# Performance work log

Measured on AMD Instinct MI355X. Metric: run time of the kernel, lower is better.

Reference implementation:

```python
import jax, jax.numpy as jnp
import numpy as np

B = 8
H_IN, W_IN = 448, 448
STRIDE = 32
NUM_CLASSES = 20
CONF_THRESH = 0.01
NMS_THRESH = 0.5
HS, WS = H_IN // STRIDE, W_IN // STRIDE  # 14, 14
N_CELLS = HS * WS  # 196
CHANNELS = [3, 64, 128, 256, 512, 512]
HEAD_OUT = 1 + NUM_CLASSES + 4  # 25


def _conv(x, w, stride):
    return jax.lax.conv_general_dilated(
        x, w, (stride, stride), 'SAME',
        dimension_numbers=('NCHW', 'OIHW', 'NCHW'))


def _create_grid():
    gy, gx = jnp.meshgrid(jnp.arange(HS), jnp.arange(WS), indexing='ij')
    return jnp.stack([gx, gy], -1).reshape(1, N_CELLS, 2).astype(jnp.float32)


def _iou_matrix(boxes):
    # boxes: [N,4] xyxy -> [N,N] pairwise IoU
    x1, y1, x2, y2 = boxes[:, 0], boxes[:, 1], boxes[:, 2], boxes[:, 3]
    area = jnp.maximum(x2 - x1, 0.0) * jnp.maximum(y2 - y1, 0.0)
    ix1 = jnp.maximum(x1[:, None], x1[None, :])
    iy1 = jnp.maximum(y1[:, None], y1[None, :])
    ix2 = jnp.minimum(x2[:, None], x2[None, :])
    iy2 = jnp.minimum(y2[:, None], y2[None, :])
    inter = jnp.maximum(ix2 - ix1, 0.0) * jnp.maximum(iy2 - iy1, 0.0)
    return inter / (area[:, None] + area[None, :] - inter + 1e-14)


def _nms_keep(scores, iou):
    # greedy per-class NMS; scores [N], iou [N,N] -> bool keep mask [N]
    order = jnp.argsort(-scores)
    iou_s = iou[order][:, order]
    idx = jnp.arange(N_CELLS)
    valid = scores[order] > CONF_THRESH

    def body(i, keep):
        sup = (iou_s[i] > NMS_THRESH) & (idx > i) & keep[i]
        return keep & (~sup)

    keep = jax.lax.fori_loop(0, N_CELLS, body, valid)
    return jnp.zeros(N_CELLS, bool).at[order].set(keep)


def setup_inputs() -> dict:
    key = jax.random.key(0)
    ks = jax.random.split(key, 8)
    x = jax.random.normal(ks[0], (B, 3, H_IN, W_IN), dtype=jnp.float32)
    params = {}
    for i in range(5):
        cin, cout = CHANNELS[i], CHANNELS[i + 1]
        std = np.sqrt(2.0 / (cin * 9))
        params[f'w{i+1}'] = jax.random.normal(ks[i + 1], (cout, cin, 3, 3), dtype=jnp.float32) * std
    std = np.sqrt(2.0 / CHANNELS[-1])
    params['w_head'] = jax.random.normal(ks[6], (HEAD_OUT, CHANNELS[-1], 1, 1), dtype=jnp.float32) * std
    return {'x': x, **params}


def reference(x, w1, w2, w3, w4, w5, w_head):
    # backbone: 5 stride-2 conv+relu stages -> stride 32
    h = x
    for w in (w1, w2, w3, w4, w5):
        h = jax.nn.relu(_conv(h, w, 2))
    pred = _conv(h, w_head, 1)                      # [B, 25, 14, 14]
    pred = pred.reshape(B, HEAD_OUT, N_CELLS).transpose(0, 2, 1)  # [B, N, 25]

    conf = jax.nn.sigmoid(pred[..., 0:1])                              # [B,N,1]
    cls_scores = jax.nn.softmax(pred[..., 1:1 + NUM_CLASSES], -1) * conf  # [B,N,C]
    txtytwth = pred[..., 1 + NUM_CLASSES:]                             # [B,N,4]

    grid = _create_grid()                                              # [1,N,2]
    xy = (jax.nn.sigmoid(txtytwth[..., :2]) + grid) * STRIDE
    wh = jnp.exp(txtytwth[..., 2:]) * STRIDE
    scale = jnp.array([W_IN, H_IN, W_IN, H_IN], dtype=jnp.float32)
    boxes = jnp.concatenate([xy - wh * 0.5, xy + wh * 0.5], -1) / scale
    boxes = jnp.clip(boxes, 0.0, 1.0)                                  # [B,N,4]

    iou = jax.vmap(_iou_matrix)(boxes)                                 # [B,N,N]
    # per-class NMS, vmapped over classes then batch
    nms_c = jax.vmap(_nms_keep, in_axes=(-1, None), out_axes=-1)       # [N,C]
    keep = jax.vmap(nms_c, in_axes=(0, 0))(cls_scores, iou)            # [B,N,C]
    final_scores = cls_scores * keep
    return jnp.concatenate([boxes, final_scores], -1)                  # [B,N,4+C]
```

## Files before the change

kernel.cpp:

```cpp
#include <hip/hip_runtime.h>
#include <math.h>

#define BATCH 8
#define NCELLS 196
#define NCLS 20
#define HEADC 25

typedef __attribute__((ext_vector_type(8))) short short8;
typedef __attribute__((ext_vector_type(4))) float f32x4;
#define MFMA16(a,b,c) __builtin_amdgcn_mfma_f32_16x16x32_bf16(a,b,c,0,0,0)

__device__ __forceinline__ unsigned short f2bf(float x) {
    union { float f; unsigned u; } a; a.f = x;
    unsigned r = a.u + 0x7FFFu + ((a.u >> 16) & 1u);
    return (unsigned short)(r >> 16);
}
__device__ __forceinline__ float bf2f(unsigned short h) {
    union { unsigned u; float f; } a; a.u = ((unsigned)h) << 16;
    return a.f;
}
__device__ __forceinline__ void split_bf(float x, unsigned short& h, unsigned short& l) {
    h = f2bf(x);
    l = f2bf(x - bf2f(h));
}

template<int CIN, int COUT>
__global__ void prep_w(const float* __restrict__ w, unsigned short* __restrict__ whi,
                       unsigned short* __restrict__ wlo) {
    constexpr int G = COUT / 16, CH = CIN / 32;
    int idx = blockIdx.x * 256 + threadIdx.x;
    if (idx >= 9 * CIN * COUT) return;
    int j    = idx & 7;
    int lane = (idx >> 3) & 63;
    int fg   = idx >> 9;
    int g    = fg % G;
    int fc   = fg / G;
    int chunk = fc % CH;
    int plane = fc / CH;
    int m = lane & 15, quad = lane >> 4;
    int co = g * 16 + m;
    int ci = chunk * 32 + quad * 8 + j;
    int ky = plane / 3, kx = plane % 3;
    float v = w[((co * CIN + ci) * 3 + ky) * 3 + kx];
    unsigned short h, l; split_bf(v, h, l);
    whi[idx] = h; wlo[idx] = l;
}

__global__ void conv1_kernel(const float* __restrict__ x, const float* __restrict__ w1,
                             unsigned short* __restrict__ ohi, unsigned short* __restrict__ olo) {
    __shared__ float sW[27][64];
    __shared__ float sX[3][3][66];
    int bid = blockIdx.x;
    int xseg = bid % 7;  bid /= 7;
    int oy   = bid % 224;
    int b    = bid / 224;
    int ox0  = xseg * 32;

    for (int e = threadIdx.x; e < 1728; e += 256) {
        int k = e >> 6, co = e & 63;
        sW[k][co] = w1[co * 27 + k];
    }
    for (int e = threadIdx.x; e < 594; e += 256) {
        int ci = e / 198;
        int r  = e - ci * 198;
        int ky = r / 66;
        int lx = r - ky * 66;
        int iy = 2 * oy + ky;
        int ix = 2 * ox0 + lx;
        float v = 0.f;
        if (lx < 65 && iy < 448 && ix < 448)
            v = x[(((size_t)b * 3 + ci) * 448 + iy) * 448 + ix];
        sX[ci][ky][lx] = v;
    }
    __syncthreads();

    int pxl = threadIdx.x >> 3;
    int cog = threadIdx.x & 7;
    float acc[8] = {0.f,0.f,0.f,0.f,0.f,0.f,0.f,0.f};
    #pragma unroll
    for (int ci = 0; ci < 3; ci++) {
        #pragma unroll
        for (int ky = 0; ky < 3; ky++) {
            const float* row = sX[ci][ky];
            #pragma unroll
            for (int kx = 0; kx < 3; kx++) {
                float iv = row[2 * pxl + kx];
                int k = (ci * 3 + ky) * 3 + kx;
                float4 wa = *(const float4*)&sW[k][cog * 8];
                float4 wb = *(const float4*)&sW[k][cog * 8 + 4];
                acc[0] += wa.x * iv; acc[1] += wa.y * iv; acc[2] += wa.z * iv; acc[3] += wa.w * iv;
                acc[4] += wb.x * iv; acc[5] += wb.y * iv; acc[6] += wb.z * iv; acc[7] += wb.w * iv;
            }
        }
    }
    union { unsigned short u[8]; uint4 v; } ph, pl;
    #pragma unroll
    for (int u = 0; u < 8; u++) {
        float v = fmaxf(acc[u], 0.f);
        split_bf(v, ph.u[u], pl.u[u]);
    }
    size_t base = ((size_t)(b * 224 + oy) * 224 + ox0 + pxl) * 64 + cog * 8;
    *(uint4*)&ohi[base] = ph.v;
    *(uint4*)&olo[base] = pl.v;
}

template<int CIN, int COUT, int HIN, int WIN, int KSPLIT, bool PARTIAL>
__launch_bounds__(256, 3)
__global__ void conv_mfma(const unsigned short* __restrict__ ahi, const unsigned short* __restrict__ alo,
                          const unsigned short* __restrict__ whi, const unsigned short* __restrict__ wlo,
                          unsigned short* __restrict__ ohi, unsigned short* __restrict__ olo,
                          float* __restrict__ part) {
    constexpr int HOUT = HIN / 2, WOUT = WIN / 2;
    constexpr int TX = (WOUT + 7) / 8, TY = (HOUT + 7) / 8;
    constexpr int COG = COUT / 128;
    constexpr int CH_TOT = CIN / 32;
    constexpr int CH = CH_TOT / KSPLIT;
    constexpr int G = COUT / 16;
    constexpr int PLANE = 17 * 17 * 36;
    constexpr size_t PSZ = (size_t)BATCH * HOUT * WOUT * COUT;

    __shared__ __align__(16) unsigned short sA[2 * PLANE];

    int bid = blockIdx.x;
    int ks  = bid % KSPLIT; bid /= KSPLIT;
    int txi = bid % TX;     bid /= TX;
    int tyi = bid % TY;     bid /= TY;
    int cg  = bid % COG;
    int b   = bid / COG;
    int oy0 = tyi * 8, ox0 = txi * 8;
    int iy0 = oy0 * 2, ix0 = ox0 * 2;

    int tid = threadIdx.x;
    int w   = tid >> 6;
    int lane = tid & 63;
    int n = lane & 15, quad = lane >> 4;

    int oyl[4], oxl[4], boff[4];
    #pragma unroll
    for (int nt = 0; nt < 4; nt++) {
        int oyq = nt >> 1, oxq = nt & 1;
        int oy_off = oyq * 4 + (n >> 2);
        int ox_off = oxq * 4 + (n & 3);
        oyl[nt] = oy0 + oy_off;
        oxl[nt] = ox0 + ox_off;
        boff[nt] = (2 * oy_off * 17 + 2 * ox_off) * 36 + quad * 8;
    }

    f32x4 zero = {0.f, 0.f, 0.f, 0.f};
    f32x4 acc[2][4];
    #pragma unroll
    for (int ct = 0; ct < 2; ct++)
        #pragma unroll
        for (int nt = 0; nt < 4; nt++) acc[ct][nt] = zero;

    int g0 = cg * 8 + w * 2;

    for (int ch = 0; ch < CH; ch++) {
        int chunk = ks * CH + ch;
        int ci0 = chunk * 32;
        __syncthreads();
        for (int e = tid; e < 17 * 17 * 8; e += 256) {
            int pxi = e >> 3, grp = e & 7;
            int liy = pxi / 17, lix = pxi - liy * 17;
            int iy = iy0 + liy, ix = ix0 + lix;
            uint4 v = make_uint4(0u, 0u, 0u, 0u);
            if (iy < HIN && ix < WIN) {
                const unsigned short* src = (grp < 4 ? ahi : alo)
                    + ((size_t)(b * HIN + iy) * WIN + ix) * CIN + ci0 + (grp & 3) * 8;
                v = *(const uint4*)src;
            }
            *(uint4*)&sA[(grp >> 2) * PLANE + pxi * 36 + (grp & 3) * 8] = v;
        }
        __syncthreads();
        #pragma unroll
        for (int pl = 0; pl < 9; pl++) {
            int ky = pl / 3, kx = pl % 3;
            size_t fbase = ((size_t)(pl * CH_TOT + chunk) * G + g0) * 512 + lane * 8;
            short8 Ah0 = *(const short8*)(whi + fbase);
            short8 Ah1 = *(const short8*)(whi + fbase + 512);
            short8 Al0 = *(const short8*)(wlo + fbase);
            short8 Al1 = *(const short8*)(wlo + fbase + 512);
            int koff = (ky * 17 + kx) * 36;
            #pragma unroll
            for (int nt = 0; nt < 4; nt++) {
                short8 Bh = *(const short8*)&sA[boff[nt] + koff];
                short8 Bl = *(const short8*)&sA[PLANE + boff[nt] + koff];
                acc[0][nt] = MFMA16(Ah0, Bh, acc[0][nt]);
                acc[0][nt] = MFMA16(Ah0, Bl, acc[0][nt]);
                acc[0][nt] = MFMA16(Al0, Bh, acc[0][nt]);
                acc[1][nt] = MFMA16(Ah1, Bh, acc[1][nt]);
                acc[1][nt] = MFMA16(Ah1, Bl, acc[1][nt]);
                acc[1][nt] = MFMA16(Al1, Bh, acc[1][nt]);
            }
        }
    }
    int cob = cg * 128 + w * 32;
    #pragma unroll
    for (int ct = 0; ct < 2; ct++) {
        #pragma unroll
        for (int nt = 0; nt < 4; nt++) {
            if (oyl[nt] >= HOUT || oxl[nt] >= WOUT) continue;
            size_t base = ((size_t)(b * HOUT + oyl[nt]) * WOUT + oxl[nt]) * COUT
                          + cob + ct * 16 + quad * 4;
            if (PARTIAL) {
                *(f32x4*)&part[(size_t)ks * PSZ + base] = acc[ct][nt];
            } else {
                unsigned long long h64 = 0ull, l64 = 0ull;
                #pragma unroll
                for (int r = 0; r < 4; r++) {
                    float v = fmaxf(acc[ct][nt][r], 0.f);
                    unsigned short hh, ll; split_bf(v, hh, ll);
                    h64 |= ((unsigned long long)hh) << (16 * r);
                    l64 |= ((unsigned long long)ll) << (16 * r);
                }
                *(unsigned long long*)&ohi[base] = h64;
                *(unsigned long long*)&olo[base] = l64;
            }
        }
    }
}

__global__ void reduce4_split(const float* __restrict__ p, unsigned short* __restrict__ oh,
                              unsigned short* __restrict__ ol) {
    const int N4 = 802816 / 4;
    int i = blockIdx.x * 256 + threadIdx.x;
    if (i >= N4) return;
    const float4* p4 = (const float4*)p;
    float4 s = p4[i];
    #pragma unroll
    for (int k = 1; k < 4; k++) {
        float4 t = p4[i + k * N4];
        s.x += t.x; s.y += t.y; s.z += t.z; s.w += t.w;
    }
    float v[4] = { fmaxf(s.x,0.f), fmaxf(s.y,0.f), fmaxf(s.z,0.f), fmaxf(s.w,0.f) };
    unsigned long long h64 = 0ull, l64 = 0ull;
    #pragma unroll
    for (int r = 0; r < 4; r++) {
        unsigned short hh, ll; split_bf(v[r], hh, ll);
        h64 |= ((unsigned long long)hh) << (16 * r);
        l64 |= ((unsigned long long)ll) << (16 * r);
    }
    *(unsigned long long*)&oh[i * 4] = h64;
    *(unsigned long long*)&ol[i * 4] = l64;
}

__global__ void head_kernel(const unsigned short* __restrict__ ah, const unsigned short* __restrict__ al,
                            const float* __restrict__ wh, float* __restrict__ pred) {
    int wave = threadIdx.x >> 6;
    int lane = threadIdx.x & 63;
    int cellid = blockIdx.x * 4 + wave;
    float acc[HEADC];
    #pragma unroll
    for (int c = 0; c < HEADC; c++) acc[c] = 0.f;
    for (int it = 0; it < 8; it++) {
        int ci = it * 64 + lane;
        size_t idx = (size_t)cellid * 512 + ci;
        float a = bf2f(ah[idx]) + bf2f(al[idx]);
        #pragma unroll
        for (int c = 0; c < HEADC; c++) acc[c] += a * wh[c * 512 + ci];
    }
    #pragma unroll
    for (int c = 0; c < HEADC; c++) {
        float v = acc[c];
        v += __shfl_down(v, 32); v += __shfl_down(v, 16); v += __shfl_down(v, 8);
        v += __shfl_down(v, 4);  v += __shfl_down(v, 2);  v += __shfl_down(v, 1);
        if (lane == 0) pred[(size_t)cellid * HEADC + c] = v;
    }
}

__global__ void decode_kernel(const float* __restrict__ pred, float* __restrict__ out,
                              float* __restrict__ cls) {
    int i = blockIdx.x * 256 + threadIdx.x;
    if (i >= BATCH * NCELLS) return;
    const float* p = pred + (size_t)i * HEADC;
    int cell = i % NCELLS;
    int gx = cell % 14, gy = cell / 14;
    float conf = 1.f / (1.f + expf(-p[0]));
    float m = p[1];
    #pragma unroll
    for (int c = 1; c < NCLS; c++) m = fmaxf(m, p[1 + c]);
    float e[NCLS], s = 0.f;
    #pragma unroll
    for (int c = 0; c < NCLS; c++) { e[c] = expf(p[1 + c] - m); s += e[c]; }
    float inv = conf / s;
    #pragma unroll
    for (int c = 0; c < NCLS; c++) cls[(size_t)i * NCLS + c] = e[c] * inv;
    float cx = (1.f / (1.f + expf(-p[21])) + gx) * 32.f;
    float cy = (1.f / (1.f + expf(-p[22])) + gy) * 32.f;
    float w  = expf(p[23]) * 32.f;
    float h  = expf(p[24]) * 32.f;
    float x1 = (cx - 0.5f * w) / 448.f, y1 = (cy - 0.5f * h) / 448.f;
    float x2 = (cx + 0.5f * w) / 448.f, y2 = (cy + 0.5f * h) / 448.f;
    x1 = fminf(fmaxf(x1, 0.f), 1.f); y1 = fminf(fmaxf(y1, 0.f), 1.f);
    x2 = fminf(fmaxf(x2, 0.f), 1.f); y2 = fminf(fmaxf(y2, 0.f), 1.f);
    float* o = out + (size_t)i * 24;
    o[0] = x1; o[1] = y1; o[2] = x2; o[3] = y2;
}

__global__ void iou_kernel(const float* __restrict__ out, float* __restrict__ iou) {
    int idx = blockIdx.x * 256 + threadIdx.x;
    if (idx >= BATCH * NCELLS * NCELLS) return;
    int j = idx % NCELLS;
    int i = (idx / NCELLS) % NCELLS;
    int b = idx / (NCELLS * NCELLS);
    const float* bi = out + (((size_t)b * NCELLS) + i) * 24;
    const float* bj = out + (((size_t)b * NCELLS) + j) * 24;
    float ai = fmaxf(bi[2] - bi[0], 0.f) * fmaxf(bi[3] - bi[1], 0.f);
    float aj = fmaxf(bj[2] - bj[0], 0.f) * fmaxf(bj[3] - bj[1], 0.f);
    float ix1 = fmaxf(bi[0], bj[0]), iy1 = fmaxf(bi[1], bj[1]);
    float ix2 = fminf(bi[2], bj[2]), iy2 = fminf(bi[3], bj[3]);
    float inter = fmaxf(ix2 - ix1, 0.f) * fmaxf(iy2 - iy1, 0.f);
    iou[idx] = inter / (ai + aj - inter + 1e-14f);
}

__global__ void nms_kernel(const float* __restrict__ cls, const float* __restrict__ iou,
                           float* __restrict__ out) {
    int b = blockIdx.x / NCLS;
    int c = blockIdx.x % NCLS;
    __shared__ float sc[NCELLS];
    __shared__ float ssort[NCELLS];
    __shared__ int   ord[NCELLS];
    __shared__ int   kp[NCELLS];
    int j = threadIdx.x;
    float sj = 0.f;
    if (j < NCELLS) {
        sj = cls[(((size_t)b * NCELLS) + j) * NCLS + c];
        sc[j] = sj;
    }
    __syncthreads();
    if (j < NCELLS) {
        int r = 0;
        for (int k = 0; k < NCELLS; k++) {
            float sk = sc[k];
            r += (sk > sj) || (sk == sj && k < j);
        }
        ord[r] = j; ssort[r] = sj; kp[r] = (sj > 0.01f) ? 1 : 0;
    }
    __syncthreads();
    int myo = (j < NCELLS) ? ord[j] : 0;
    const float* iob = iou + (size_t)b * NCELLS * NCELLS;
    for (int i = 0; i < NCELLS; i++) {
        __syncthreads();
        if (!kp[i]) continue;
        if (j > i && j < NCELLS && kp[j]) {
            if (iob[ord[i] * NCELLS + myo] > 0.5f) kp[j] = 0;
        }
    }
    __syncthreads();
    if (j < NCELLS)
        out[(((size_t)b * NCELLS) + ord[j]) * 24 + 4 + c] = kp[j] ? ssort[j] : 0.f;
}

extern "C" void kernel_launch(void* const* d_in, const int* in_sizes, int n_in,
                              void* d_out, int out_size, void* d_ws, size_t ws_size,
                              hipStream_t stream) {
    const float* x  = (const float*)d_in[0];
    const float* w1 = (const float*)d_in[1];
    const float* w2 = (const float*)d_in[2];
    const float* w3 = (const float*)d_in[3];
    const float* w4 = (const float*)d_in[4];
    const float* w5 = (const float*)d_in[5];
    const float* wh = (const float*)d_in[6];
    float* out = (float*)d_out;
    char* base = (char*)d_ws;

    unsigned short* a1h = (unsigned short*)(base);
    unsigned short* a1l = a1h + 25690112;
    unsigned short* a3h = (unsigned short*)(base);
    unsigned short* a3l = a3h + 6422528;
    float*          part5 = (float*)(base);
    unsigned short* a5h = (unsigned short*)(base + 12845056);
    unsigned short* a5l = a5h + 802816;
    float* pred = (float*)(base + 16056320);
    float* clsb = (float*)(base + 16213120);
    float* ioub = (float*)(base + 16338560);
    unsigned short* a2h = (unsigned short*)(base + 102760448);
    unsigned short* a2l = a2h + 12845056;
    unsigned short* a4h = (unsigned short*)(base + 102760448);
    unsigned short* a4l = a4h + 3211264;
    unsigned short* w2h = (unsigned short*)(base + 154140672);
    unsigned short* w3h = w2h + 73728;
    unsigned short* w4h = w3h + 294912;
    unsigned short* w5h = w4h + 1179648;
    unsigned short* w2l = (unsigned short*)(base + 161955840);
    unsigned short* w3l = w2l + 73728;
    unsigned short* w4l = w3l + 294912;
    unsigned short* w5l = w4l + 1179648;

    prep_w<64, 128> <<<288,  256, 0, stream>>>(w2, w2h, w2l);
    prep_w<128, 256><<<1152, 256, 0, stream>>>(w3, w3h, w3l);
    prep_w<256, 512><<<4608, 256, 0, stream>>>(w4, w4h, w4l);
    prep_w<512, 512><<<9216, 256, 0, stream>>>(w5, w5h, w5l);

    conv1_kernel<<<12544, 256, 0, stream>>>(x, w1, a1h, a1l);

    conv_mfma<64, 128, 224, 224, 1, false><<<1568, 256, 0, stream>>>(
        a1h, a1l, w2h, w2l, a2h, a2l, nullptr);
    conv_mfma<128, 256, 112, 112, 1, false><<<784, 256, 0, stream>>>(
        a2h, a2l, w3h, w3l, a3h, a3l, nullptr);
    conv_mfma<256, 512, 56, 56, 1, false><<<512, 256, 0, stream>>>(
        a3h, a3l, w4h, w4l, a4h, a4l, nullptr);
    conv_mfma<512, 512, 28, 28, 4, true><<<512, 256, 0, stream>>>(
        a4h, a4l, w5h, w5l, nullptr, nullptr, part5);
    reduce4_split<<<784, 256, 0, stream>>>(part5, a5h, a5l);

    head_kernel<<<392, 256, 0, stream>>>(a5h, a5l, wh, pred);
    decode_kernel<<<7, 256, 0, stream>>>(pred, out, clsb);
    iou_kernel<<<1201, 256, 0, stream>>>(out, ioub);
    nms_kernel<<<160, 256, 0, stream>>>(clsb, ioub, out);
}
```

Baseline: 516.1 us.

## Swizzle LDS layout, raise occupancy, and add split-K to conv4 and conv5

Replaces the padded 36-element-per-pixel LDS layout with a dense 32-element layout and XOR-swizzles the 16-byte chunks to avoid bank conflicts. This shrinks shared memory, which lets launch bounds go from 3 to 4 blocks per CU. Conv4 now uses split-K by 2 with a new reduction kernel, and conv5 goes from split-K 4 to 8, doubling the grids to fill more CUs. The price is extra fp32 partial-sum traffic and extra reduction launches. The workspace offsets are rearranged to fit the larger partial buffers.

```diff
diff --git a/kernel.cpp b/kernel.cpp
--- a/kernel.cpp
+++ b/kernel.cpp
@@ -105,7 +105,7 @@
 }
 
 template<int CIN, int COUT, int HIN, int WIN, int KSPLIT, bool PARTIAL>
-__launch_bounds__(256, 3)
+__launch_bounds__(256, 4)
 __global__ void conv_mfma(const unsigned short* __restrict__ ahi, const unsigned short* __restrict__ alo,
                           const unsigned short* __restrict__ whi, const unsigned short* __restrict__ wlo,
                           unsigned short* __restrict__ ohi, unsigned short* __restrict__ olo,
@@ -116,10 +116,10 @@
     constexpr int CH_TOT = CIN / 32;
     constexpr int CH = CH_TOT / KSPLIT;
     constexpr int G = COUT / 16;
-    constexpr int PLANE = 17 * 17 * 36;
+    constexpr int PLANE_E = 17 * 17 * 32;
     constexpr size_t PSZ = (size_t)BATCH * HOUT * WOUT * COUT;
 
-    __shared__ __align__(16) unsigned short sA[2 * PLANE];
+    __shared__ __align__(16) unsigned short sA[2 * PLANE_E];
 
     int bid = blockIdx.x;
     int ks  = bid % KSPLIT; bid /= KSPLIT;
@@ -135,7 +135,7 @@
     int lane = tid & 63;
     int n = lane & 15, quad = lane >> 4;
 
-    int oyl[4], oxl[4], boff[4];
+    int oyl[4], oxl[4], pbase[4];
     #pragma unroll
     for (int nt = 0; nt < 4; nt++) {
         int oyq = nt >> 1, oxq = nt & 1;
@@ -143,7 +143,7 @@
         int ox_off = oxq * 4 + (n & 3);
         oyl[nt] = oy0 + oy_off;
         oxl[nt] = ox0 + ox_off;
-        boff[nt] = (2 * oy_off * 17 + 2 * ox_off) * 36 + quad * 8;
+        pbase[nt] = 2 * oy_off * 17 + 2 * ox_off;
     }
 
     f32x4 zero = {0.f, 0.f, 0.f, 0.f};
@@ -165,11 +165,12 @@
             int iy = iy0 + liy, ix = ix0 + lix;
             uint4 v = make_uint4(0u, 0u, 0u, 0u);
             if (iy < HIN && ix < WIN) {
-                const unsigned short* src = (grp < 4 ? ahi : alo)
+                const unsigned short* src = ((grp & 4) ? alo : ahi)
                     + ((size_t)(b * HIN + iy) * WIN + ix) * CIN + ci0 + (grp & 3) * 8;
                 v = *(const uint4*)src;
             }
-            *(uint4*)&sA[(grp >> 2) * PLANE + pxi * 36 + (grp & 3) * 8] = v;
+            int u = pxi * 4 + ((grp & 3) ^ ((pxi >> 1) & 3));
+            *(uint4*)&sA[((grp >> 2) ? PLANE_E : 0) + u * 8] = v;
         }
         __syncthreads();
         #pragma unroll
@@ -180,11 +181,13 @@
             short8 Ah1 = *(const short8*)(whi + fbase + 512);
             short8 Al0 = *(const short8*)(wlo + fbase);
             short8 Al1 = *(const short8*)(wlo + fbase + 512);
-            int koff = (ky * 17 + kx) * 36;
+            int dp = ky * 17 + kx;
             #pragma unroll
             for (int nt = 0; nt < 4; nt++) {
-                short8 Bh = *(const short8*)&sA[boff[nt] + koff];
-                short8 Bl = *(const short8*)&sA[PLANE + boff[nt] + koff];
+                int p = pbase[nt] + dp;
+                int u = p * 4 + (quad ^ ((p >> 1) & 3));
+                short8 Bh = *(const short8*)&sA[u * 8];
+                short8 Bl = *(const short8*)&sA[PLANE_E + u * 8];
                 acc[0][nt] = MFMA16(Ah0, Bh, acc[0][nt]);
                 acc[0][nt] = MFMA16(Ah0, Bl, acc[0][nt]);
                 acc[0][nt] = MFMA16(Al0, Bh, acc[0][nt]);
@@ -220,16 +223,17 @@
     }
 }
 
-__global__ void reduce4_split(const float* __restrict__ p, unsigned short* __restrict__ oh,
-                              unsigned short* __restrict__ ol) {
-    const int N4 = 802816 / 4;
+template<int KS>
+__global__ void reduceN_split(const float* __restrict__ p, unsigned short* __restrict__ oh,
+                              unsigned short* __restrict__ ol, int n) {
+    int n4 = n >> 2;
     int i = blockIdx.x * 256 + threadIdx.x;
-    if (i >= N4) return;
+    if (i >= n4) return;
     const float4* p4 = (const float4*)p;
     float4 s = p4[i];
     #pragma unroll
-    for (int k = 1; k < 4; k++) {
-        float4 t = p4[i + k * N4];
+    for (int k = 1; k < KS; k++) {
+        float4 t = p4[i + (size_t)k * n4];
         s.x += t.x; s.y += t.y; s.z += t.z; s.w += t.w;
     }
     float v[4] = { fmaxf(s.x,0.f), fmaxf(s.y,0.f), fmaxf(s.z,0.f), fmaxf(s.w,0.f) };
@@ -368,12 +372,13 @@
     unsigned short* a1l = a1h + 25690112;
     unsigned short* a3h = (unsigned short*)(base);
     unsigned short* a3l = a3h + 6422528;
-    float*          part5 = (float*)(base);
-    unsigned short* a5h = (unsigned short*)(base + 12845056);
+    float* part4 = (float*)(base + 25690112);
+    float* part5 = (float*)(base);
+    unsigned short* a5h = (unsigned short*)(base + 51380224);
     unsigned short* a5l = a5h + 802816;
-    float* pred = (float*)(base + 16056320);
-    float* clsb = (float*)(base + 16213120);
-    float* ioub = (float*)(base + 16338560);
+    float* pred = (float*)(base + 54589440);
+    float* clsb = (float*)(base + 54746240);
+    float* ioub = (float*)(base + 54871680);
     unsigned short* a2h = (unsigned short*)(base + 102760448);
     unsigned short* a2l = a2h + 12845056;
     unsigned short* a4h = (unsigned short*)(base + 102760448);
@@ -398,11 +403,12 @@
         a1h, a1l, w2h, w2l, a2h, a2l, nullptr);
     conv_mfma<128, 256, 112, 112, 1, false><<<784, 256, 0, stream>>>(
         a2h, a2l, w3h, w3l, a3h, a3l, nullptr);
-    conv_mfma<256, 512, 56, 56, 1, false><<<512, 256, 0, stream>>>(
-        a3h, a3l, w4h, w4l, a4h, a4l, nullptr);
-    conv_mfma<512, 512, 28, 28, 4, true><<<512, 256, 0, stream>>>(
+    conv_mfma<256, 512, 56, 56, 2, true><<<1024, 256, 0, stream>>>(
+        a3h, a3l, w4h, w4l, nullptr, nullptr, part4);
+    reduceN_split<2><<<3136, 256, 0, stream>>>(part4, a4h, a4l, 3211264);
+    conv_mfma<512, 512, 28, 28, 8, true><<<1024, 256, 0, stream>>>(
         a4h, a4l, w5h, w5l, nullptr, nullptr, part5);
-    reduce4_split<<<784, 256, 0, stream>>>(part5, a5h, a5l);
+    reduceN_split<8><<<784, 256, 0, stream>>>(part5, a5h, a5l, 802816);
 
     head_kernel<<<392, 256, 0, stream>>>(a5h, a5l, wh, pred);
     decode_kernel<<<7, 256, 0, stream>>>(pred, out, clsb);
```

Result: faster. 468.7 us (-9.2%).
